# Kernel optimization log

Measured on AMD Instinct MI355X. Metric: run time of the kernel, lower is better.

Reference implementation:

```python
import jax, jax.numpy as jnp
import numpy as np

F = 256          # in_features
T = 8            # num_fragment_ion_types = 4 types * 2 charges
N_MONO, N_CLEAV, N_FRAG, N_OUT = 150000, 100000, 80000, 40000
D_CLEAV, D_JOIN, D_COMB = 4, 2, 4


def setup_inputs() -> dict:
    key = jax.random.key(0)
    ks = jax.random.split(key, 14)
    s = 0.05
    return {
        "feature": jax.random.normal(ks[0], (N_MONO, F), jnp.float32),
        "Wg_lost": jax.random.normal(ks[1], (F, 1), jnp.float32) * s,
        "Wg_ret": jax.random.normal(ks[2], (F, 1), jnp.float32) * s,
        "W_ih": jax.random.normal(ks[3], (4 * F, 2 * F), jnp.float32) * s,
        "W_hh": jax.random.normal(ks[4], (4 * F, F), jnp.float32) * s,
        "b_ih": jax.random.normal(ks[5], (4 * F,), jnp.float32) * s,
        "b_hh": jax.random.normal(ks[6], (4 * F,), jnp.float32) * s,
        "Wg_frag": jax.random.normal(ks[7], (F, 1), jnp.float32) * s,
        "W_out": jax.random.normal(ks[8], (F, T), jnp.float32) * s,
        "b_out": jnp.zeros((T,), jnp.float32),
        "lost_src": jax.random.randint(ks[9], (N_CLEAV, D_CLEAV), 0, N_MONO),
        "retained_src": jax.random.randint(ks[10], (N_CLEAV, D_CLEAV), 0, N_MONO),
        "join_src": jax.random.randint(ks[11], (N_FRAG, D_JOIN), 0, N_CLEAV),
        "combine_src": jax.random.randint(ks[12], (N_OUT, D_COMB), 0, N_FRAG),
    }


def _attention_sum(h, Wg):
    # h: [N, D, F] mailbox; gate = Linear(F,1,no bias); softmax over neighbor axis
    logits = jnp.einsum('ndf,fo->ndo', h, Wg)          # [N, D, 1]
    a = jax.nn.softmax(logits, axis=1)
    return jnp.sum(a * h, axis=1)                       # [N, F]


def _lstm(x, W_ih, W_hh, b_ih, b_hh):
    # x: [N, L, I]; torch nn.LSTM gate order i,f,g,o; zero initial state
    N = x.shape[0]
    H = W_hh.shape[1]
    def step(carry, xt):
        h, c = carry
        gates = xt @ W_ih.T + h @ W_hh.T + b_ih + b_hh  # [N, 4H]
        i, f, g, o = jnp.split(gates, 4, axis=-1)
        c = jax.nn.sigmoid(f) * c + jax.nn.sigmoid(i) * jnp.tanh(g)
        h = jax.nn.sigmoid(o) * jnp.tanh(c)
        return (h, c), h
    init = (jnp.zeros((N, H), x.dtype), jnp.zeros((N, H), x.dtype))
    _, hs = jax.lax.scan(step, init, jnp.swapaxes(x, 0, 1))
    return jnp.swapaxes(hs, 0, 1)                       # [N, L, H]


def reference(feature, Wg_lost, Wg_ret, W_ih, W_hh, b_ih, b_hh,
              Wg_frag, W_out, b_out,
              lost_src, retained_src, join_src, combine_src):
    h_lost = _attention_sum(feature[lost_src], Wg_lost)        # [N_cleav, F]
    h_ret = _attention_sum(feature[retained_src], Wg_ret)      # [N_cleav, F]
    cleav = jnp.concatenate([h_lost, h_ret], axis=-1)          # [N_cleav, 2F]
    # Fragment pull over 'join' edges: LSTM over neighbor set, then attention sum
    hs = _lstm(cleav[join_src], W_ih, W_hh, b_ih, b_hh)        # [N_frag, D_join, F]
    frag = _attention_sum(hs, Wg_frag)                         # [N_frag, F]
    # Output head: Linear + ReLU
    frag_out = jax.nn.relu(frag @ W_out + b_out)               # [N_frag, T]
    # copy_u_sum over 'combine' edges: scatter-sum of src outputs to dst
    return frag_out[combine_src].sum(axis=1)                   # [N_out, T]
```

## Files before the change

kernel.cpp:

```cpp
#include <hip/hip_runtime.h>

typedef unsigned short u16;
typedef unsigned int u32;
typedef float f32x4 __attribute__((ext_vector_type(4)));
typedef __bf16 bf16x8 __attribute__((ext_vector_type(8)));

#define F 256
#define T_OUT 8
#define N_MONO 150000
#define N_CLEAV 100000
#define N_FRAG 80000
#define N_FRAG_PAD 80128
#define N_OUT 40000
#define M_CLEAV_PAD 100352

static __device__ __forceinline__ u16 f2bf(float f) {
  u32 u = __float_as_uint(f);
  u32 r = (u + 0x7FFFu + ((u >> 16) & 1u)) >> 16;
  return (u16)r;
}
static __device__ __forceinline__ float bf2f(u16 b) {
  return __uint_as_float(((u32)b) << 16);
}
static __device__ __forceinline__ float sigmoidf(float x) {
  return __frcp_rn(1.0f + __expf(-x));
}
static __device__ __forceinline__ float fast_tanh(float x) {
  return 1.0f - 2.0f * __frcp_rn(__expf(2.0f * x) + 1.0f);
}
static __device__ __forceinline__ void async_copy16(const u16* g, const u16* l) {
  __builtin_amdgcn_global_load_lds(
      (const __attribute__((address_space(1))) u32*)g,
      (__attribute__((address_space(3))) u32*)l,
      16, 0, 0);
}

__global__ __launch_bounds__(256) void feat_prep(
    const float* __restrict__ feat, const float* __restrict__ WgL,
    const float* __restrict__ WgR, u16* __restrict__ featb,
    float* __restrict__ glog,
    const float* __restrict__ Wih, const float* __restrict__ Whh,
    const float* __restrict__ bih, const float* __restrict__ bhh,
    u16* __restrict__ Wihb, u16* __restrict__ Whhb, float* __restrict__ bias) {
  int i = blockIdx.x * 256 + threadIdx.x;
  if (i < 1024 * 512) {
    Wihb[i] = f2bf(Wih[i]);
    if (i < 1024 * 256) Whhb[i] = f2bf(Whh[i]);
    if (i < 1024) bias[i] = bih[i] + bhh[i];
  }
  int wave = threadIdx.x >> 6, lane = threadIdx.x & 63;
  int n = blockIdx.x * 4 + wave;
  if (n >= N_MONO) return;
  float4 x = *(const float4*)(feat + (size_t)n * F + lane * 4);
  u32 lo = (u32)f2bf(x.x) | ((u32)f2bf(x.y) << 16);
  u32 hi = (u32)f2bf(x.z) | ((u32)f2bf(x.w) << 16);
  *(uint2*)(featb + (size_t)n * F + lane * 4) = make_uint2(lo, hi);
  float4 wl = *(const float4*)(WgL + lane * 4);
  float4 wr = *(const float4*)(WgR + lane * 4);
  float pl = x.x * wl.x + x.y * wl.y + x.z * wl.z + x.w * wl.w;
  float pr = x.x * wr.x + x.y * wr.y + x.z * wr.z + x.w * wr.w;
#pragma unroll
  for (int off = 32; off; off >>= 1) {
    pl += __shfl_xor(pl, off);
    pr += __shfl_xor(pr, off);
  }
  if (lane == 0) {
    glog[n * 2] = pl;
    glog[n * 2 + 1] = pr;
  }
}

__global__ __launch_bounds__(256) void attn_pull2(
    const u16* __restrict__ featb, const float* __restrict__ glog,
    const int* __restrict__ lostS, const int* __restrict__ retS,
    u16* __restrict__ cleav) {
  int wave = threadIdx.x >> 6, lane = threadIdx.x & 63;
  int n = blockIdx.x * 4 + wave;
  if (n >= N_CLEAV) return;
#pragma unroll
  for (int sg = 0; sg < 2; ++sg) {
    const int* src = sg ? retS : lostS;
    int4 ridx = *(const int4*)(src + n * 4);
    int r[4] = {ridx.x, ridx.y, ridx.z, ridx.w};
    ushort4 x4[4];
    float lg[4];
#pragma unroll
    for (int d = 0; d < 4; ++d) {
      x4[d] = *(const ushort4*)(featb + (size_t)r[d] * F + lane * 4);
      lg[d] = glog[r[d] * 2 + sg];
    }
    float mx = fmaxf(fmaxf(lg[0], lg[1]), fmaxf(lg[2], lg[3]));
    float e0 = __expf(lg[0] - mx), e1 = __expf(lg[1] - mx);
    float e2 = __expf(lg[2] - mx), e3 = __expf(lg[3] - mx);
    float inv = __frcp_rn(e0 + e1 + e2 + e3);
    float a[4] = {e0 * inv, e1 * inv, e2 * inv, e3 * inv};
    float acc[4] = {0.f, 0.f, 0.f, 0.f};
#pragma unroll
    for (int d = 0; d < 4; ++d) {
      const u16* xp = (const u16*)&x4[d];
#pragma unroll
      for (int k = 0; k < 4; k++) acc[k] += a[d] * bf2f(xp[k]);
    }
    u32 lo = (u32)f2bf(acc[0]) | ((u32)f2bf(acc[1]) << 16);
    u32 hi = (u32)f2bf(acc[2]) | ((u32)f2bf(acc[3]) << 16);
    *(uint2*)(cleav + (size_t)n * 512 + sg * 256 + lane * 4) = make_uint2(lo, hi);
  }
}

template <int EPI, int K, int BM>
__global__ __launch_bounds__(512, 2) void gemm256(
    const u16* __restrict__ A, const u16* __restrict__ Bw,
    u16* __restrict__ C, const float* __restrict__ bias,
    const int* __restrict__ join, const u16* __restrict__ P,
    const u16* __restrict__ c1, const float* __restrict__ Wg,
    u16* __restrict__ h2s, float* __restrict__ p2p,
    int nper, int mstrips_valid) {
  constexpr int AREG = BM * 64;
  constexpr int BSZ = AREG + 16384;
  constexpr int WMH = BM / 2;
  constexpr int IB = BM / 32;
  constexpr int IB_HI = IB - 4;
  __shared__ u16 sh[2][BSZ];
  const int flat = blockIdx.x;
  const int xcd = flat & 7;
  const int w = flat >> 3;
  const int mstrip = xcd * nper + (w >> 2);
  const int nstrip = w & 3;
  if (mstrip >= mstrips_valid) return;
  const int m0 = mstrip * BM;
  const int n0 = nstrip * 256;

  const int tid = threadIdx.x;
  const int lane = tid & 63;
  const int wave = tid >> 6;
  const int quad = lane >> 4;
  const int l16 = lane & 15;
  const int s7 = l16 & 7;
  const int wm2 = wave >> 2;
  const int wn4 = wave & 3;

  const int arow = (wm2 * WMH + l16) * 64;
  const int brow = AREG + (wn4 * 64 + l16) * 64;
  const int coff0 = (quad ^ s7) * 8;
  const int coff1 = ((4 + quad) ^ s7) * 8;

  int sr[4], sw[4], dwv[4], bsrc[4];
#pragma unroll
  for (int r = 0; r < 4; r++) {
    int c = r * 512 + tid;
    int row = c >> 3;
    sr[r] = row;
    sw[r] = ((c & 7) ^ (row & 7)) * 8;
    dwv[r] = (r * 512 + (tid & ~63)) * 8;
    bsrc[r] = (EPI == 1)
        ? ((row >> 4) & 3) * 256 + nstrip * 64 + ((row >> 6) << 4) + (row & 15)
        : n0 + row;
  }
  const u16* Abase = A + (size_t)m0 * K;

  auto stageA = [&](int buf, int kt, int h) {
#pragma unroll
    for (int rr = 0; rr < 2; rr++) {
      int r = 2 * h + rr;
      if (r * 512 + tid < BM * 8)
        async_copy16(Abase + (size_t)sr[r] * K + kt * 64 + sw[r], &sh[buf][dwv[r]]);
    }
  };
  auto stageB = [&](int buf, int kt, int h) {
#pragma unroll
    for (int rr = 0; rr < 2; rr++) {
      int r = 2 * h + rr;
      async_copy16(Bw + (size_t)bsrc[r] * K + kt * 64 + sw[r], &sh[buf][AREG + dwv[r]]);
    }
  };

  f32x4 acc[IB][4];
#pragma unroll
  for (int i = 0; i < IB; i++)
#pragma unroll
    for (int j = 0; j < 4; j++) acc[i][j] = (f32x4){0.f, 0.f, 0.f, 0.f};

  constexpr int nK = K / 64;
  stageA(0, 0, 0); stageA(0, 0, 1); stageB(0, 0, 0); stageB(0, 0, 1);
  if (nK > 1) { stageB(1, 1, 0); stageB(1, 1, 1); }
  __builtin_amdgcn_s_waitcnt(0xF74);
  __builtin_amdgcn_s_barrier();

  bf16x8 a[4][2], b0[2][2], b1[2][2];
#pragma unroll
  for (int t = 0; t < nK; ++t) {
    const int bsel = t & 1;
    const u16* S = &sh[bsel][0];

#pragma unroll
    for (int i = 0; i < 4; i++) {
      a[i][0] = *(const bf16x8*)&S[arow + i * 1024 + coff0];
      a[i][1] = *(const bf16x8*)&S[arow + i * 1024 + coff1];
    }
#pragma unroll
    for (int j = 0; j < 2; j++) {
      b0[j][0] = *(const bf16x8*)&S[brow + j * 1024 + coff0];
      b0[j][1] = *(const bf16x8*)&S[brow + j * 1024 + coff1];
    }
    if (t + 1 < nK) stageA(bsel ^ 1, t + 1, 0);
    __builtin_amdgcn_s_waitcnt(0xC87F);
    __builtin_amdgcn_s_barrier();
    __builtin_amdgcn_s_waitcnt(0xC07F);
    __builtin_amdgcn_sched_barrier(0);
    __builtin_amdgcn_s_setprio(1);
#pragma unroll
    for (int i = 0; i < 4; i++)
#pragma unroll
      for (int j = 0; j < 2; j++) {
        acc[i][j] = __builtin_amdgcn_mfma_f32_16x16x32_bf16(a[i][0], b0[j][0], acc[i][j], 0, 0, 0);
        acc[i][j] = __builtin_amdgcn_mfma_f32_16x16x32_bf16(a[i][1], b0[j][1], acc[i][j], 0, 0, 0);
      }
    __builtin_amdgcn_s_setprio(0);
    __builtin_amdgcn_s_barrier();

#pragma unroll
    for (int j = 0; j < 2; j++) {
      b1[j][0] = *(const bf16x8*)&S[brow + (2 + j) * 1024 + coff0];
      b1[j][1] = *(const bf16x8*)&S[brow + (2 + j) * 1024 + coff1];
    }
    if (t + 1 < nK) stageA(bsel ^ 1, t + 1, 1);
    __builtin_amdgcn_s_barrier();
    __builtin_amdgcn_s_waitcnt(0xC07F);
    __builtin_amdgcn_sched_barrier(0);
    __builtin_amdgcn_s_setprio(1);
#pragma unroll
    for (int i = 0; i < 4; i++)
#pragma unroll
      for (int j = 0; j < 2; j++) {
        acc[i][2 + j] = __builtin_amdgcn_mfma_f32_16x16x32_bf16(a[i][0], b1[j][0], acc[i][2 + j], 0, 0, 0);
        acc[i][2 + j] = __builtin_amdgcn_mfma_f32_16x16x32_bf16(a[i][1], b1[j][1], acc[i][2 + j], 0, 0, 0);
      }
    __builtin_amdgcn_s_setprio(0);
    __builtin_amdgcn_s_barrier();

#pragma unroll
    for (int i = 0; i < IB_HI; i++) {
      a[i][0] = *(const bf16x8*)&S[arow + (4 + i) * 1024 + coff0];
      a[i][1] = *(const bf16x8*)&S[arow + (4 + i) * 1024 + coff1];
    }
    if (t + 2 < nK) stageB(bsel, t + 2, 0);
    __builtin_amdgcn_s_barrier();
    __builtin_amdgcn_s_waitcnt(0xC07F);
    __builtin_amdgcn_sched_barrier(0);
    __builtin_amdgcn_s_setprio(1);
#pragma unroll
    for (int i = 0; i < IB_HI; i++)
#pragma unroll
      for (int j = 0; j < 2; j++) {
        acc[4 + i][j] = __builtin_amdgcn_mfma_f32_16x16x32_bf16(a[i][0], b0[j][0], acc[4 + i][j], 0, 0, 0);
        acc[4 + i][j] = __builtin_amdgcn_mfma_f32_16x16x32_bf16(a[i][1], b0[j][1], acc[4 + i][j], 0, 0, 0);
      }
    __builtin_amdgcn_s_setprio(0);
    __builtin_amdgcn_s_barrier();

    if (t + 2 < nK) stageB(bsel, t + 2, 1);
    __builtin_amdgcn_s_barrier();
    __builtin_amdgcn_s_setprio(1);
#pragma unroll
    for (int i = 0; i < IB_HI; i++)
#pragma unroll
      for (int j = 0; j < 2; j++) {
        acc[4 + i][2 + j] = __builtin_amdgcn_mfma_f32_16x16x32_bf16(a[i][0], b1[j][0], acc[4 + i][2 + j], 0, 0, 0);
        acc[4 + i][2 + j] = __builtin_amdgcn_mfma_f32_16x16x32_bf16(a[i][1], b1[j][1], acc[4 + i][2 + j], 0, 0, 0);
      }
    __builtin_amdgcn_s_setprio(0);
    if (t + 2 < nK) __builtin_amdgcn_s_waitcnt(0xF74);
    else            __builtin_amdgcn_s_waitcnt(0xF70);
    __builtin_amdgcn_s_barrier();
  }

  if constexpr (EPI == 0) {
    float badd[4];
#pragma unroll
    for (int j = 0; j < 4; j++)
      badd[j] = bias[n0 + wn4 * 64 + j * 16 + l16];
#pragma unroll
    for (int i = 0; i < IB; i++) {
      const int mrow = m0 + wm2 * WMH + i * 16 + quad * 4;
#pragma unroll
      for (int j = 0; j < 4; j++) {
        const int n = n0 + wn4 * 64 + j * 16 + l16;
#pragma unroll
        for (int r = 0; r < 4; r++)
          C[(size_t)(mrow + r) * 1024 + n] = f2bf(acc[i][j][r] + badd[j]);
      }
    }
  } else {
    const int hg = nstrip * 64 + wn4 * 16 + l16;
    const float wgv = Wg[hg];
#pragma unroll
    for (int i = 0; i < IB; i++) {
#pragma unroll
      for (int r = 0; r < 4; r++) {
        const int m = m0 + wm2 * WMH + i * 16 + quad * 4 + r;
        const int j1 = (m < N_FRAG) ? join[2 * m + 1] : 0;
        const u16* prow = P + (size_t)j1 * 1024 + hg;
        float gi = acc[i][0][r] + bf2f(prow[0]);
        float gf = acc[i][1][r] + bf2f(prow[256]);
        float gg = acc[i][2][r] + bf2f(prow[512]);
        float go = acc[i][3][r] + bf2f(prow[768]);
        float c1v = bf2f(c1[(size_t)m * 256 + hg]);
        float c2 = sigmoidf(gf) * c1v + sigmoidf(gi) * fast_tanh(gg);
        float h2 = sigmoidf(go) * fast_tanh(c2);
        float p = h2 * wgv;
        p += __shfl_xor(p, 1); p += __shfl_xor(p, 2);
        p += __shfl_xor(p, 4); p += __shfl_xor(p, 8);
        if (l16 == 0) p2p[(size_t)m * 16 + nstrip * 4 + wn4] = p;
        h2s[((size_t)nstrip * N_FRAG_PAD + m) * 64 + wn4 * 16 + l16] = f2bf(h2);
      }
    }
  }
}

__global__ __launch_bounds__(256) void lstm_step1(
    const u16* __restrict__ P, const int* __restrict__ join,
    const float* __restrict__ Wg, u16* __restrict__ h1,
    u16* __restrict__ c1, float* __restrict__ p1) {
  int wave = threadIdx.x >> 6, lane = threadIdx.x & 63;
  int m = blockIdx.x * 4 + wave;
  if (m >= N_FRAG) return;
  int j0 = join[2 * m];
  const u16* row = P + (size_t)j0 * 1024 + lane * 4;
  ushort4 iv = *(const ushort4*)(row);
  ushort4 gv = *(const ushort4*)(row + 512);
  ushort4 ov = *(const ushort4*)(row + 768);
  float4 wg = *(const float4*)(Wg + lane * 4);
  const u16* ivp = (const u16*)&iv;
  const u16* gvp = (const u16*)&gv;
  const u16* ovp = (const u16*)&ov;
  const float* wgp = (const float*)&wg;
  ushort4 h4, c4;
  u16* h4p = (u16*)&h4;
  u16* c4p = (u16*)&c4;
  float pl = 0.f;
#pragma unroll
  for (int k = 0; k < 4; k++) {
    float c = sigmoidf(bf2f(ivp[k])) * fast_tanh(bf2f(gvp[k]));
    float hv = sigmoidf(bf2f(ovp[k])) * fast_tanh(c);
    h4p[k] = f2bf(hv);
    c4p[k] = f2bf(c);
    pl += bf2f(h4p[k]) * wgp[k];
  }
#pragma unroll
  for (int off = 32; off; off >>= 1) pl += __shfl_xor(pl, off);
  *(ushort4*)(h1 + (size_t)m * 256 + lane * 4) = h4;
  *(ushort4*)(c1 + (size_t)m * 256 + lane * 4) = c4;
  if (lane == 0) p1[m] = pl;
}

__global__ __launch_bounds__(256) void lstm_attn_out(
    const u16* __restrict__ h1, const u16* __restrict__ h2s,
    const float* __restrict__ p1, const float* __restrict__ p2p,
    const float* __restrict__ Wout, const float* __restrict__ bout,
    float* __restrict__ frag_out) {
  int wave = threadIdx.x >> 6, lane = threadIdx.x & 63;
  int m = blockIdx.x * 4 + wave;
  if (m >= N_FRAG) return;
  float4 q = *(const float4*)(p2p + (size_t)m * 16 + (lane & 3) * 4);
  float p2 = q.x + q.y + q.z + q.w;
  p2 += __shfl_xor(p2, 1);
  p2 += __shfl_xor(p2, 2);
  float p1v = p1[m];
  float mx = fmaxf(p1v, p2);
  float e1 = __expf(p1v - mx), e2 = __expf(p2 - mx);
  float inv = __frcp_rn(e1 + e2);
  float a1 = e1 * inv, a2 = e2 * inv;

  ushort4 h1v = *(const ushort4*)(h1 + (size_t)m * 256 + lane * 4);
  ushort4 h2v = *(const ushort4*)(h2s + ((size_t)(lane >> 4) * N_FRAG_PAD + m) * 64 + (lane & 15) * 4);
  const u16* h1p = (const u16*)&h1v;
  const u16* h2p = (const u16*)&h2v;

  float acc[8];
#pragma unroll
  for (int t = 0; t < 8; t++) acc[t] = 0.f;
#pragma unroll
  for (int k = 0; k < 4; k++) {
    float frag = a1 * bf2f(h1p[k]) + a2 * bf2f(h2p[k]);
    int h = lane * 4 + k;
    float4 w0 = *(const float4*)(Wout + h * 8);
    float4 w1 = *(const float4*)(Wout + h * 8 + 4);
    acc[0] += frag * w0.x; acc[1] += frag * w0.y;
    acc[2] += frag * w0.z; acc[3] += frag * w0.w;
    acc[4] += frag * w1.x; acc[5] += frag * w1.y;
    acc[6] += frag * w1.z; acc[7] += frag * w1.w;
  }
#pragma unroll
  for (int off = 32; off; off >>= 1)
#pragma unroll
    for (int t = 0; t < 8; t++) acc[t] += __shfl_xor(acc[t], off);
  if (lane == 0) {
    float4 o0, o1;
    o0.x = fmaxf(acc[0] + bout[0], 0.f);
    o0.y = fmaxf(acc[1] + bout[1], 0.f);
    o0.z = fmaxf(acc[2] + bout[2], 0.f);
    o0.w = fmaxf(acc[3] + bout[3], 0.f);
    o1.x = fmaxf(acc[4] + bout[4], 0.f);
    o1.y = fmaxf(acc[5] + bout[5], 0.f);
    o1.z = fmaxf(acc[6] + bout[6], 0.f);
    o1.w = fmaxf(acc[7] + bout[7], 0.f);
    *(float4*)(frag_out + (size_t)m * 8) = o0;
    *(float4*)(frag_out + (size_t)m * 8 + 4) = o1;
  }
}

__global__ __launch_bounds__(256) void scatter_sum(
    const float* __restrict__ frag_out, const int* __restrict__ comb,
    float* __restrict__ out) {
  int tid = blockIdx.x * 256 + threadIdx.x;
  if (tid >= N_OUT * 8) return;
  int n = tid >> 3, t = tid & 7;
  float s = 0.f;
#pragma unroll
  for (int d = 0; d < 4; d++) {
    int f = comb[n * 4 + d];
    s += frag_out[(size_t)f * 8 + t];
  }
  out[tid] = s;
}

extern "C" void kernel_launch(void* const* d_in, const int* in_sizes, int n_in,
                              void* d_out, int out_size, void* d_ws, size_t ws_size,
                              hipStream_t stream) {
  const float* feature = (const float*)d_in[0];
  const float* WgL = (const float*)d_in[1];
  const float* WgR = (const float*)d_in[2];
  const float* Wih = (const float*)d_in[3];
  const float* Whh = (const float*)d_in[4];
  const float* bih = (const float*)d_in[5];
  const float* bhh = (const float*)d_in[6];
  const float* Wgf = (const float*)d_in[7];
  const float* Wout = (const float*)d_in[8];
  const float* bout = (const float*)d_in[9];
  const int* lostS = (const int*)d_in[10];
  const int* retS = (const int*)d_in[11];
  const int* joinS = (const int*)d_in[12];
  const int* combS = (const int*)d_in[13];
  float* out = (float*)d_out;

  char* ws = (char*)d_ws;
  size_t off = 0;
  auto alloc = [&](size_t bytes) -> char* {
    char* p = ws + off;
    off = (off + bytes + 255) & ~(size_t)255;
    return p;
  };
  u16* Wihb = (u16*)alloc((size_t)1024 * 512 * 2);
  u16* Whhb = (u16*)alloc((size_t)1024 * 256 * 2);
  float* bias = (float*)alloc(1024 * 4);
  u16* P = (u16*)alloc((size_t)M_CLEAV_PAD * 1024 * 2);
  u16* h1 = (u16*)alloc((size_t)N_FRAG_PAD * 256 * 2);
  u16* c1 = (u16*)alloc((size_t)N_FRAG_PAD * 256 * 2);
  u16* h2s = (u16*)alloc((size_t)4 * N_FRAG_PAD * 64 * 2);
  float* p2p = (float*)alloc((size_t)N_FRAG_PAD * 16 * 4);
  float* p1 = (float*)alloc((size_t)N_FRAG_PAD * 4);
  float* frag_out = (float*)alloc((size_t)N_FRAG * 8 * 4);
  u16* cleav = (u16*)alloc((size_t)M_CLEAV_PAD * 1024 * 2);
  u16* featb = P;
  float* glog = (float*)(P + (size_t)N_MONO * F);

  feat_prep<<<(N_MONO + 3) / 4, 256, 0, stream>>>(
      feature, WgL, WgR, featb, glog, Wih, Whh, bih, bhh, Wihb, Whhb, bias);
  attn_pull2<<<N_CLEAV / 4, 256, 0, stream>>>(featb, glog, lostS, retS, cleav);
  gemm256<0, 512, 224><<<1792, 512, 0, stream>>>(
      cleav, Wihb, P, bias, nullptr, nullptr, nullptr, nullptr, nullptr, nullptr,
      56, 448);
  lstm_step1<<<N_FRAG / 4, 256, 0, stream>>>(P, joinS, Wgf, h1, c1, p1);
  gemm256<1, 256, 256><<<1280, 512, 0, stream>>>(
      h1, Whhb, nullptr, nullptr, joinS, P, c1, Wgf, h2s, p2p,
      40, 313);
  lstm_attn_out<<<N_FRAG / 4, 256, 0, stream>>>(
      h1, h2s, p1, p2p, Wout, bout, frag_out);
  scatter_sum<<<(N_OUT * 8 + 255) / 256, 256, 0, stream>>>(frag_out, combS, out);
}
```

Measured before the change: 772.1 us.

## Fuse join gather into per-fragment LSTM GEMMs and drop the cleavage projection buffer

Replaces the precomputed input projection over all cleavage nodes, and its gathers, with two fragment-level GEMMs. These load cleav rows directly through join indices. The second GEMM concatenates the x and h operands along K=768, and the step-1 LSTM cell and attention logit partials move into the first GEMM's epilogue. This removes the large bf16 P buffer's write and its scattered re-reads, plus a separate elementwise kernel. In exchange it recomputes the x projection per fragment edge rather than per cleavage node, which adds substantial MFMA work, including forget-gate columns that step 0 never uses.

```diff
diff --git a/kernel.cpp b/kernel.cpp
--- a/kernel.cpp
+++ b/kernel.cpp
@@ -12,7 +12,6 @@
 #define N_FRAG 80000
 #define N_FRAG_PAD 80128
 #define N_OUT 40000
-#define M_CLEAV_PAD 100352
 
 static __device__ __forceinline__ u16 f2bf(float f) {
   u32 u = __float_as_uint(f);
@@ -107,19 +106,17 @@
   }
 }
 
-template <int EPI, int K, int BM>
-__global__ __launch_bounds__(512, 2) void gemm256(
-    const u16* __restrict__ A, const u16* __restrict__ Bw,
-    u16* __restrict__ C, const float* __restrict__ bias,
-    const int* __restrict__ join, const u16* __restrict__ P,
-    const u16* __restrict__ c1, const float* __restrict__ Wg,
-    u16* __restrict__ h2s, float* __restrict__ p2p,
+template <int STEP, int K>
+__global__ __launch_bounds__(512, 2) void gemm_frag(
+    const u16* __restrict__ cleavA, const u16* __restrict__ h1A,
+    const u16* __restrict__ Wihb, const u16* __restrict__ Whhb,
+    const int* __restrict__ join, const float* __restrict__ bias,
+    const u16* __restrict__ c1in, const float* __restrict__ Wg,
+    u16* __restrict__ h1out, u16* __restrict__ c1out, u16* __restrict__ h2s,
+    float* __restrict__ pp,
     int nper, int mstrips_valid) {
-  constexpr int AREG = BM * 64;
+  constexpr int AREG = 256 * 64;
   constexpr int BSZ = AREG + 16384;
-  constexpr int WMH = BM / 2;
-  constexpr int IB = BM / 32;
-  constexpr int IB_HI = IB - 4;
   __shared__ u16 sh[2][BSZ];
   const int flat = blockIdx.x;
   const int xcd = flat & 7;
@@ -127,8 +124,7 @@
   const int mstrip = xcd * nper + (w >> 2);
   const int nstrip = w & 3;
   if (mstrip >= mstrips_valid) return;
-  const int m0 = mstrip * BM;
-  const int n0 = nstrip * 256;
+  const int m0 = mstrip * 256;
 
   const int tid = threadIdx.x;
   const int lane = tid & 63;
@@ -139,12 +135,12 @@
   const int wm2 = wave >> 2;
   const int wn4 = wave & 3;
 
-  const int arow = (wm2 * WMH + l16) * 64;
+  const int arow = (wm2 * 128 + l16) * 64;
   const int brow = AREG + (wn4 * 64 + l16) * 64;
   const int coff0 = (quad ^ s7) * 8;
   const int coff1 = ((4 + quad) ^ s7) * 8;
 
-  int sr[4], sw[4], dwv[4], bsrc[4];
+  int sr[4], sw[4], dwv[4], bsrc[4], jidx[4];
 #pragma unroll
   for (int r = 0; r < 4; r++) {
     int c = r * 512 + tid;
@@ -152,31 +148,40 @@
     sr[r] = row;
     sw[r] = ((c & 7) ^ (row & 7)) * 8;
     dwv[r] = (r * 512 + (tid & ~63)) * 8;
-    bsrc[r] = (EPI == 1)
-        ? ((row >> 4) & 3) * 256 + nstrip * 64 + ((row >> 6) << 4) + (row & 15)
-        : n0 + row;
-  }
-  const u16* Abase = A + (size_t)m0 * K;
+    bsrc[r] = ((row >> 4) & 3) * 256 + nstrip * 64 + ((row >> 6) << 4) + (row & 15);
+    int m = m0 + row;
+    int mi = m < N_FRAG ? m : N_FRAG - 1;
+    jidx[r] = join[2 * mi + STEP];
+  }
 
   auto stageA = [&](int buf, int kt, int h) {
 #pragma unroll
     for (int rr = 0; rr < 2; rr++) {
       int r = 2 * h + rr;
-      if (r * 512 + tid < BM * 8)
-        async_copy16(Abase + (size_t)sr[r] * K + kt * 64 + sw[r], &sh[buf][dwv[r]]);
+      const u16* src;
+      if (STEP == 1 && kt >= 8)
+        src = h1A + (size_t)(m0 + sr[r]) * 256 + (kt - 8) * 64 + sw[r];
+      else
+        src = cleavA + (size_t)jidx[r] * 512 + kt * 64 + sw[r];
+      async_copy16(src, &sh[buf][dwv[r]]);
     }
   };
   auto stageB = [&](int buf, int kt, int h) {
 #pragma unroll
     for (int rr = 0; rr < 2; rr++) {
       int r = 2 * h + rr;
-      async_copy16(Bw + (size_t)bsrc[r] * K + kt * 64 + sw[r], &sh[buf][AREG + dwv[r]]);
+      const u16* src;
+      if (STEP == 1 && kt >= 8)
+        src = Whhb + (size_t)bsrc[r] * 256 + (kt - 8) * 64 + sw[r];
+      else
+        src = Wihb + (size_t)bsrc[r] * 512 + kt * 64 + sw[r];
+      async_copy16(src, &sh[buf][AREG + dwv[r]]);
     }
   };
 
-  f32x4 acc[IB][4];
-#pragma unroll
-  for (int i = 0; i < IB; i++)
+  f32x4 acc[8][4];
+#pragma unroll
+  for (int i = 0; i < 8; i++)
 #pragma unroll
     for (int j = 0; j < 4; j++) acc[i][j] = (f32x4){0.f, 0.f, 0.f, 0.f};
 
@@ -239,7 +244,7 @@
     __builtin_amdgcn_s_barrier();
 
 #pragma unroll
-    for (int i = 0; i < IB_HI; i++) {
+    for (int i = 0; i < 4; i++) {
       a[i][0] = *(const bf16x8*)&S[arow + (4 + i) * 1024 + coff0];
       a[i][1] = *(const bf16x8*)&S[arow + (4 + i) * 1024 + coff1];
     }
@@ -249,7 +254,7 @@
     __builtin_amdgcn_sched_barrier(0);
     __builtin_amdgcn_s_setprio(1);
 #pragma unroll
-    for (int i = 0; i < IB_HI; i++)
+    for (int i = 0; i < 4; i++)
 #pragma unroll
       for (int j = 0; j < 2; j++) {
         acc[4 + i][j] = __builtin_amdgcn_mfma_f32_16x16x32_bf16(a[i][0], b0[j][0], acc[4 + i][j], 0, 0, 0);
@@ -262,7 +267,7 @@
     __builtin_amdgcn_s_barrier();
     __builtin_amdgcn_s_setprio(1);
 #pragma unroll
-    for (int i = 0; i < IB_HI; i++)
+    for (int i = 0; i < 4; i++)
 #pragma unroll
       for (int j = 0; j < 2; j++) {
         acc[4 + i][2 + j] = __builtin_amdgcn_mfma_f32_16x16x32_bf16(a[i][0], b1[j][0], acc[4 + i][2 + j], 0, 0, 0);
@@ -274,100 +279,59 @@
     __builtin_amdgcn_s_barrier();
   }
 
-  if constexpr (EPI == 0) {
-    float badd[4];
-#pragma unroll
-    for (int j = 0; j < 4; j++)
-      badd[j] = bias[n0 + wn4 * 64 + j * 16 + l16];
-#pragma unroll
-    for (int i = 0; i < IB; i++) {
-      const int mrow = m0 + wm2 * WMH + i * 16 + quad * 4;
-#pragma unroll
-      for (int j = 0; j < 4; j++) {
-        const int n = n0 + wn4 * 64 + j * 16 + l16;
-#pragma unroll
-        for (int r = 0; r < 4; r++)
-          C[(size_t)(mrow + r) * 1024 + n] = f2bf(acc[i][j][r] + badd[j]);
+  const int hg = nstrip * 64 + wn4 * 16 + l16;
+  const float bI = bias[hg];
+  const float bF = bias[256 + hg];
+  const float bG = bias[512 + hg];
+  const float bO = bias[768 + hg];
+  const float wgv = Wg[hg];
+#pragma unroll
+  for (int i = 0; i < 8; i++) {
+#pragma unroll
+    for (int r = 0; r < 4; r++) {
+      const int m = m0 + wm2 * 128 + i * 16 + quad * 4 + r;
+      float gi = acc[i][0][r] + bI;
+      float gg = acc[i][2][r] + bG;
+      float go = acc[i][3][r] + bO;
+      float hv;
+      if (STEP == 0) {
+        float cv = sigmoidf(gi) * fast_tanh(gg);
+        hv = sigmoidf(go) * fast_tanh(cv);
+        h1out[(size_t)m * 256 + hg] = f2bf(hv);
+        c1out[(size_t)m * 256 + hg] = f2bf(cv);
+      } else {
+        float gf = acc[i][1][r] + bF;
+        float c1v = bf2f(c1in[(size_t)m * 256 + hg]);
+        float cv = sigmoidf(gf) * c1v + sigmoidf(gi) * fast_tanh(gg);
+        hv = sigmoidf(go) * fast_tanh(cv);
+        h2s[((size_t)nstrip * N_FRAG_PAD + m) * 64 + wn4 * 16 + l16] = f2bf(hv);
       }
-    }
-  } else {
-    const int hg = nstrip * 64 + wn4 * 16 + l16;
-    const float wgv = Wg[hg];
-#pragma unroll
-    for (int i = 0; i < IB; i++) {
-#pragma unroll
-      for (int r = 0; r < 4; r++) {
-        const int m = m0 + wm2 * WMH + i * 16 + quad * 4 + r;
-        const int j1 = (m < N_FRAG) ? join[2 * m + 1] : 0;
-        const u16* prow = P + (size_t)j1 * 1024 + hg;
-        float gi = acc[i][0][r] + bf2f(prow[0]);
-        float gf = acc[i][1][r] + bf2f(prow[256]);
-        float gg = acc[i][2][r] + bf2f(prow[512]);
-        float go = acc[i][3][r] + bf2f(prow[768]);
-        float c1v = bf2f(c1[(size_t)m * 256 + hg]);
-        float c2 = sigmoidf(gf) * c1v + sigmoidf(gi) * fast_tanh(gg);
-        float h2 = sigmoidf(go) * fast_tanh(c2);
-        float p = h2 * wgv;
-        p += __shfl_xor(p, 1); p += __shfl_xor(p, 2);
-        p += __shfl_xor(p, 4); p += __shfl_xor(p, 8);
-        if (l16 == 0) p2p[(size_t)m * 16 + nstrip * 4 + wn4] = p;
-        h2s[((size_t)nstrip * N_FRAG_PAD + m) * 64 + wn4 * 16 + l16] = f2bf(h2);
-      }
-    }
-  }
-}
-
-__global__ __launch_bounds__(256) void lstm_step1(
-    const u16* __restrict__ P, const int* __restrict__ join,
-    const float* __restrict__ Wg, u16* __restrict__ h1,
-    u16* __restrict__ c1, float* __restrict__ p1) {
-  int wave = threadIdx.x >> 6, lane = threadIdx.x & 63;
-  int m = blockIdx.x * 4 + wave;
-  if (m >= N_FRAG) return;
-  int j0 = join[2 * m];
-  const u16* row = P + (size_t)j0 * 1024 + lane * 4;
-  ushort4 iv = *(const ushort4*)(row);
-  ushort4 gv = *(const ushort4*)(row + 512);
-  ushort4 ov = *(const ushort4*)(row + 768);
-  float4 wg = *(const float4*)(Wg + lane * 4);
-  const u16* ivp = (const u16*)&iv;
-  const u16* gvp = (const u16*)&gv;
-  const u16* ovp = (const u16*)&ov;
-  const float* wgp = (const float*)&wg;
-  ushort4 h4, c4;
-  u16* h4p = (u16*)&h4;
-  u16* c4p = (u16*)&c4;
-  float pl = 0.f;
-#pragma unroll
-  for (int k = 0; k < 4; k++) {
-    float c = sigmoidf(bf2f(ivp[k])) * fast_tanh(bf2f(gvp[k]));
-    float hv = sigmoidf(bf2f(ovp[k])) * fast_tanh(c);
-    h4p[k] = f2bf(hv);
-    c4p[k] = f2bf(c);
-    pl += bf2f(h4p[k]) * wgp[k];
-  }
-#pragma unroll
-  for (int off = 32; off; off >>= 1) pl += __shfl_xor(pl, off);
-  *(ushort4*)(h1 + (size_t)m * 256 + lane * 4) = h4;
-  *(ushort4*)(c1 + (size_t)m * 256 + lane * 4) = c4;
-  if (lane == 0) p1[m] = pl;
+      float p = bf2f(f2bf(hv)) * wgv;
+      p += __shfl_xor(p, 1); p += __shfl_xor(p, 2);
+      p += __shfl_xor(p, 4); p += __shfl_xor(p, 8);
+      if (l16 == 0) pp[(size_t)m * 16 + nstrip * 4 + wn4] = p;
+    }
+  }
 }
 
 __global__ __launch_bounds__(256) void lstm_attn_out(
     const u16* __restrict__ h1, const u16* __restrict__ h2s,
-    const float* __restrict__ p1, const float* __restrict__ p2p,
+    const float* __restrict__ p1p, const float* __restrict__ p2p,
     const float* __restrict__ Wout, const float* __restrict__ bout,
     float* __restrict__ frag_out) {
   int wave = threadIdx.x >> 6, lane = threadIdx.x & 63;
   int m = blockIdx.x * 4 + wave;
   if (m >= N_FRAG) return;
-  float4 q = *(const float4*)(p2p + (size_t)m * 16 + (lane & 3) * 4);
-  float p2 = q.x + q.y + q.z + q.w;
+  float4 q2 = *(const float4*)(p2p + (size_t)m * 16 + (lane & 3) * 4);
+  float p2 = q2.x + q2.y + q2.z + q2.w;
   p2 += __shfl_xor(p2, 1);
   p2 += __shfl_xor(p2, 2);
-  float p1v = p1[m];
-  float mx = fmaxf(p1v, p2);
-  float e1 = __expf(p1v - mx), e2 = __expf(p2 - mx);
+  float4 q1 = *(const float4*)(p1p + (size_t)m * 16 + (lane & 3) * 4);
+  float p1 = q1.x + q1.y + q1.z + q1.w;
+  p1 += __shfl_xor(p1, 1);
+  p1 += __shfl_xor(p1, 2);
+  float mx = fmaxf(p1, p2);
+  float e1 = __expf(p1 - mx), e2 = __expf(p2 - mx);
   float inv = __frcp_rn(e1 + e2);
   float a1 = e1 * inv, a2 = e2 * inv;
 
@@ -453,28 +417,26 @@
   u16* Wihb = (u16*)alloc((size_t)1024 * 512 * 2);
   u16* Whhb = (u16*)alloc((size_t)1024 * 256 * 2);
   float* bias = (float*)alloc(1024 * 4);
-  u16* P = (u16*)alloc((size_t)M_CLEAV_PAD * 1024 * 2);
+  u16* featb = (u16*)alloc((size_t)N_MONO * F * 2);
+  float* glog = (float*)alloc((size_t)N_MONO * 2 * 4);
+  u16* cleav = (u16*)alloc((size_t)N_CLEAV * 512 * 2);
   u16* h1 = (u16*)alloc((size_t)N_FRAG_PAD * 256 * 2);
   u16* c1 = (u16*)alloc((size_t)N_FRAG_PAD * 256 * 2);
   u16* h2s = (u16*)alloc((size_t)4 * N_FRAG_PAD * 64 * 2);
+  float* p1p = (float*)alloc((size_t)N_FRAG_PAD * 16 * 4);
   float* p2p = (float*)alloc((size_t)N_FRAG_PAD * 16 * 4);
-  float* p1 = (float*)alloc((size_t)N_FRAG_PAD * 4);
   float* frag_out = (float*)alloc((size_t)N_FRAG * 8 * 4);
-  u16* cleav = (u16*)alloc((size_t)M_CLEAV_PAD * 1024 * 2);
-  u16* featb = P;
-  float* glog = (float*)(P + (size_t)N_MONO * F);
 
   feat_prep<<<(N_MONO + 3) / 4, 256, 0, stream>>>(
       feature, WgL, WgR, featb, glog, Wih, Whh, bih, bhh, Wihb, Whhb, bias);
   attn_pull2<<<N_CLEAV / 4, 256, 0, stream>>>(featb, glog, lostS, retS, cleav);
-  gemm256<0, 512, 224><<<1792, 512, 0, stream>>>(
-      cleav, Wihb, P, bias, nullptr, nullptr, nullptr, nullptr, nullptr, nullptr,
-      56, 448);
-  lstm_step1<<<N_FRAG / 4, 256, 0, stream>>>(P, joinS, Wgf, h1, c1, p1);
-  gemm256<1, 256, 256><<<1280, 512, 0, stream>>>(
-      h1, Whhb, nullptr, nullptr, joinS, P, c1, Wgf, h2s, p2p,
-      40, 313);
+  gemm_frag<0, 512><<<1280, 512, 0, stream>>>(
+      cleav, nullptr, Wihb, Whhb, joinS, bias, nullptr, Wgf,
+      h1, c1, nullptr, p1p, 40, 313);
+  gemm_frag<1, 768><<<1280, 512, 0, stream>>>(
+      cleav, h1, Wihb, Whhb, joinS, bias, c1, Wgf,
+      nullptr, nullptr, h2s, p2p, 40, 313);
   lstm_attn_out<<<N_FRAG / 4, 256, 0, stream>>>(
-      h1, h2s, p1, p2p, Wout, bout, frag_out);
+      h1, h2s, p1p, p2p, Wout, bout, frag_out);
   scatter_sum<<<(N_OUT * 8 + 255) / 256, 256, 0, stream>>>(frag_out, combS, out);
 }
```

New measurement: 729.4 us. 5.5% less time.
